# Performance work log

Measured on AMD Instinct MI355X. Metric: run time of the kernel, lower is better.

The kernel has to match this reference:

```python
import math
import jax, jax.numpy as jnp
import numpy as np

N_TOKENS = 2048
HIDDEN = 2880
HEAD_DIM = 64
N_HEADS = 64          # total attention heads
N_KV = 8              # key/value heads
Q_MULT = N_HEADS // N_KV
SLIDING_WINDOW = 128  # layer_idx=0 (even) -> window active
ROPE_BASE = 150000.0
INIT_CTX = 4096.0
ROPE_SCALE = 32.0
NTK_ALPHA = 1.0
NTK_BETA = 32.0
QKV_DIM = HEAD_DIM * (N_HEADS + 2 * N_KV)  # 5120
EPS = 1e-5
NEG = -1e30


def _cos_sin(n_tokens):
    # YaRN-scaled rotary tables (scaling_factor > 1 branch)
    freq = ROPE_BASE ** (jnp.arange(0, HEAD_DIM, 2, dtype=jnp.float32) / HEAD_DIM)
    concentration = 0.1 * jnp.log(jnp.float32(ROPE_SCALE)) + 1.0
    d_half = HEAD_DIM / 2
    log_base = jnp.log(jnp.float32(ROPE_BASE))
    low = d_half * jnp.log(jnp.float32(INIT_CTX / (NTK_BETA * 2 * np.pi))) / log_base
    high = d_half * jnp.log(jnp.float32(INIT_CTX / (NTK_ALPHA * 2 * np.pi))) / log_base
    interpolation = 1.0 / (ROPE_SCALE * freq)
    extrapolation = 1.0 / freq
    ramp = (jnp.arange(d_half, dtype=jnp.float32) - low) / (high - low)
    mask = 1.0 - jnp.clip(ramp, 0.0, 1.0)
    inv_freq = interpolation * (1.0 - mask) + extrapolation * mask
    t = jnp.arange(n_tokens, dtype=jnp.float32)
    freqs = t[:, None] * inv_freq[None, :]          # [n, head_dim//2]
    return jnp.cos(freqs) * concentration, jnp.sin(freqs) * concentration


def _apply_rotary(x, cos, sin):
    # x: [n, heads, head_dim]; cos/sin: [n, head_dim//2]
    cos = cos[:, None, :].astype(x.dtype)
    sin = sin[:, None, :].astype(x.dtype)
    x1, x2 = jnp.split(x, 2, axis=-1)
    return jnp.concatenate((x1 * cos - x2 * sin, x2 * cos + x1 * sin), axis=-1)


def _rmsnorm(x, scale):
    t = x.astype(jnp.float32)
    rms = jnp.sqrt(jnp.mean(t * t, axis=-1, keepdims=True) + EPS)
    return (t / rms * scale).astype(x.dtype)


def _sdpa(q, k, v, sinks):
    # q: [n, h_kv, q_mult, d]; k, v: [n, h_kv, d]; sinks: [n_heads]
    n = q.shape[0]
    sm_scale = 1.0 / math.sqrt(HEAD_DIM)
    q32, k32, v32 = q.astype(jnp.float32), k.astype(jnp.float32), v.astype(jnp.float32)
    qk = jnp.einsum('qhmd,khd->hmqk', q32, k32) * jnp.float32(sm_scale)
    i = jnp.arange(n)
    # causal AND within sliding window: q - window < k <= q
    allowed = (i[None, :] <= i[:, None]) & (i[None, :] > i[:, None] - SLIDING_WINDOW)
    qk = qk + jnp.where(allowed, jnp.float32(0.0), jnp.float32(NEG))[None, None, :, :]
    s = sinks.astype(jnp.float32).reshape(N_KV, Q_MULT, 1, 1)
    s = jnp.broadcast_to(s, (N_KV, Q_MULT, n, 1))
    w = jax.nn.softmax(jnp.concatenate([qk, s], axis=-1), axis=-1)[..., :-1]
    attn = jnp.einsum('hmqk,khd->qhmd', w, v32)
    return attn.astype(q.dtype).reshape(n, -1)  # [n, n_heads*head_dim]


def setup_inputs() -> dict:
    key = jax.random.key(0)
    ks = jax.random.split(key, 5)
    s = 0.02
    return {
        'x': jax.random.normal(ks[0], (N_TOKENS, HIDDEN), jnp.float32),
        'norm_scale': jnp.ones((HIDDEN,), jnp.float32),
        'w_qkv': jax.random.normal(ks[1], (HIDDEN, QKV_DIM), jnp.float32) * s,
        'b_qkv': jnp.zeros((QKV_DIM,), jnp.float32),
        'sinks': jax.random.normal(ks[2], (N_HEADS,), jnp.float32),
        'w_out': jax.random.normal(ks[3], (N_HEADS * HEAD_DIM, HIDDEN), jnp.float32) * s,
        'b_out': jnp.zeros((HIDDEN,), jnp.float32),
    }


def reference(x, norm_scale, w_qkv, b_qkv, sinks, w_out, b_out):
    n = x.shape[0]
    t = _rmsnorm(x, norm_scale)
    qkv = t @ w_qkv + b_qkv                                   # [n, qkv_dim]
    q_end = N_HEADS * HEAD_DIM
    k_end = q_end + N_KV * HEAD_DIM
    q = qkv[:, :q_end].reshape(n, N_KV, Q_MULT, HEAD_DIM)
    k = qkv[:, q_end:k_end].reshape(n, N_KV, HEAD_DIM)
    v = qkv[:, k_end:].reshape(n, N_KV, HEAD_DIM)
    cos, sin = _cos_sin(n)
    q = _apply_rotary(q.reshape(n, -1, HEAD_DIM), cos, sin).reshape(n, N_KV, Q_MULT, HEAD_DIM)
    k = _apply_rotary(k, cos, sin)
    attn = _sdpa(q, k, v, sinks)                              # [n, n_heads*head_dim]
    return x + (attn @ w_out + b_out)
```

## Files before the change

### kernel.cpp

```cpp
#include <hip/hip_runtime.h>
#include <hip/hip_bf16.h>
#include <math.h>

#define N_TOK 2048
#define HIDDEN 2880
#define QKV_DIM 5120
#define LOG2E 1.44269504088896340736f

typedef __attribute__((ext_vector_type(8))) short short8;
typedef __attribute__((ext_vector_type(4))) float f32x4;
typedef __attribute__((ext_vector_type(16))) float f32x16;

__device__ __forceinline__ float bf2f(unsigned short u) {
  union { unsigned int i; float f; } c; c.i = ((unsigned int)u) << 16; return c.f;
}
__device__ __forceinline__ unsigned short f2bf(float f) {
  union { float f; unsigned int i; } c; c.f = f;
  unsigned int i = c.i;
  return (unsigned short)((i + 0x7FFFu + ((i >> 16) & 1u)) >> 16);
}
__device__ __forceinline__ void gload16(const void* g, void* l) {
  __builtin_amdgcn_global_load_lds((const __attribute__((address_space(1))) void*)g,
                                   (__attribute__((address_space(3))) void*)l, 16, 0, 0);
}

__global__ __launch_bounds__(256) void prep1_kernel(
    const float* __restrict__ w_qkv, unsigned short* __restrict__ wqkvT,
    const float* __restrict__ x, const float* __restrict__ scale,
    unsigned short* __restrict__ t_bf,
    float* __restrict__ cstab, float* __restrict__ sntab)
{
  __shared__ float tile[64][65];
  int b = blockIdx.x;
  const int t = threadIdx.x;
  if (b >= 5648) {
    const float log_base = 11.9183905731f;
    const float low  = 32.f * logf(4096.f / (32.f * 6.283185307179586f)) / log_base;
    const float high = 32.f * logf(4096.f / 6.283185307179586f) / log_base;
    const float conc = 1.3465735903f;
    int e0 = (b - 5648) * 1024 + t * 4;
#pragma unroll
    for (int k = 0; k < 4; ++k) {
      int entry = e0 + k;
      int token = entry >> 5, d = entry & 31;
      float fj = (float)d;
      float extrap = expf(-log_base * fj * 0.03125f);
      float interp = extrap * 0.03125f;
      float ramp = (fj - low) / (high - low);
      float maskv = 1.f - fminf(fmaxf(ramp, 0.f), 1.f);
      float inv_freq = interp * (1.f - maskv) + extrap * maskv;
      float ang = (float)token * inv_freq;
      float s, c;
      sincosf(ang, &s, &c);
      cstab[entry] = c * conc;
      sntab[entry] = s * conc;
    }
    return;
  }
  if (b >= 3600) {
    int row = b - 3600;
    const float* xr = x + (size_t)row * HIDDEN;
    float ss = 0.f;
    for (int i = t; i < HIDDEN / 4; i += 256) {
      float4 v = ((const float4*)xr)[i];
      ss += v.x * v.x + v.y * v.y + v.z * v.z + v.w * v.w;
    }
#pragma unroll
    for (int off = 32; off; off >>= 1) ss += __shfl_down(ss, off, 64);
    __shared__ float red[4];
    if ((t & 63) == 0) red[t >> 6] = ss;
    __syncthreads();
    float total = red[0] + red[1] + red[2] + red[3];
    float rinv = rsqrtf(total / (float)HIDDEN + 1e-5f);
    for (int i = t; i < HIDDEN / 4; i += 256) {
      float4 v = ((const float4*)xr)[i];
      float4 s4 = ((const float4*)scale)[i];
      union { unsigned short u[4]; uint2 p; } pk;
      pk.u[0] = f2bf(v.x * rinv * s4.x);
      pk.u[1] = f2bf(v.y * rinv * s4.y);
      pk.u[2] = f2bf(v.z * rinv * s4.z);
      pk.u[3] = f2bf(v.w * rinv * s4.w);
      *(uint2*)&t_bf[(size_t)row * HIDDEN + i * 4] = pk.p;
    }
    return;
  }
  int bx = b % 80, by = b / 80;
  const int r0 = by * 64, c0 = bx * 64;
  const int c4 = t & 15, rr = t >> 4;
#pragma unroll
  for (int p = 0; p < 4; ++p) {
    int row = rr + p * 16;
    float4 v = *(const float4*)&w_qkv[(size_t)(r0 + row) * 5120 + c0 + c4 * 4];
    tile[row][c4 * 4 + 0] = v.x; tile[row][c4 * 4 + 1] = v.y;
    tile[row][c4 * 4 + 2] = v.z; tile[row][c4 * 4 + 3] = v.w;
  }
  __syncthreads();
  const int rc = t & 7;
#pragma unroll
  for (int it = 0; it < 2; ++it) {
    int cc = (t >> 3) + it * 32;
    unsigned short tmp[8];
#pragma unroll
    for (int i = 0; i < 8; ++i) tmp[i] = f2bf(tile[rc * 8 + i][cc]);
    *(uint4*)&wqkvT[(size_t)(c0 + cc) * 2880 + r0 + rc * 8] = *(uint4*)tmp;
  }
}

template <int NF, int EPI>
__global__ __launch_bounds__(512, 2) void gemm8(
    const unsigned short* __restrict__ A,
    const unsigned short* __restrict__ Bt,
    const float* __restrict__ bias,
    const float* __restrict__ resid,
    void* __restrict__ Cout,
    int K, int Ncols)
{
  constexpr int BUFSZ = 16384 + NF * 8192;
  constexpr int NCH = 2 + NF;
  constexpr int HALF = NCH / 2;
  __shared__ char smem_[2 * BUFSZ];
  const int tid = threadIdx.x;
  const int lane = tid & 63;
  const int w = tid >> 6;
  const int fr = lane & 15, fq = lane >> 4;
  const int wr = w >> 2, wc = w & 3;

  const int nwg = gridDim.x;
  const int cpx = nwg >> 3;
  const int wg = (blockIdx.x & 7) * cpx + (blockIdx.x >> 3);
  const int by = wg & 15, bx = wg >> 4;
  const int row0 = by * 128, col0 = bx * (NF * 64);

  const unsigned short* gsrc[NCH];
  int ldsoff[NCH];
#pragma unroll
  for (int c = 0; c < NCH; ++c) {
    int g = tid + 512 * c;
    if (g < 1024) {
      int kk = g >> 9, rr = (g >> 2) & 127, u = g & 3;
      gsrc[c] = A + (size_t)(row0 + rr) * K + kk * 32 + ((u ^ ((rr >> 1) & 3)) * 8);
      ldsoff[c] = kk * 8192 + rr * 64 + u * 16;
    } else {
      int g2 = g - 1024;
      int kk = g2 / (NF * 256);
      int rm = g2 - kk * (NF * 256);
      int rr = rm >> 2, u = rm & 3;
      gsrc[c] = Bt + (size_t)(col0 + rr) * K + kk * 32 + ((u ^ ((rr >> 1) & 3)) * 8);
      ldsoff[c] = 16384 + kk * (NF * 4096) + rr * 64 + u * 16;
    }
  }
  const int urd = (fq ^ ((fr >> 1) & 3)) * 16;
  const int aoffb = (wr * 64 + fr) * 64 + urd;
  const int boffb = 16384 + (wc * NF * 16 + fr) * 64 + urd;

  f32x4 acc[4][NF];
#pragma unroll
  for (int mf = 0; mf < 4; ++mf)
#pragma unroll
    for (int nf = 0; nf < NF; ++nf) acc[mf][nf] = (f32x4)0.f;

  const int NT = K >> 6;

#define ISSUE(c) gload16(gsrc[c] + ktn, smem_ + nbufo + ldsoff[c])
#define RD_A(mf, kk) (*(const short8*)(smem_ + bufo + (kk)*8192 + (mf)*1024 + aoffb))
#define RD_B(nf, kk) (*(const short8*)(smem_ + bufo + (kk)*(NF*4096) + (nf)*1024 + boffb))

  {
    const int ktn = 0, nbufo = 0;
#pragma unroll
    for (int c = 0; c < NCH; ++c) gload16(gsrc[c] + ktn, smem_ + nbufo + ldsoff[c]);
  }

  for (int t = 0; t < NT; ++t) {
    const int bufo = (t & 1) * BUFSZ;
    const int nbufo = bufo ^ BUFSZ;
    const int ktn = (t + 1) * 64;
    const bool pref = (t + 1) < NT;

    asm volatile("s_waitcnt vmcnt(0)" ::: "memory");
    __builtin_amdgcn_s_barrier();

    if (pref) {
#pragma unroll
      for (int c = 0; c < HALF; ++c) ISSUE(c);
    }

    short8 afr[4], bfr[NF];
#pragma unroll
    for (int nf = 0; nf < NF; ++nf) bfr[nf] = RD_B(nf, 0);
#pragma unroll
    for (int mf = 0; mf < 4; ++mf) afr[mf] = RD_A(mf, 0);
    __builtin_amdgcn_s_setprio(1);
#pragma unroll
    for (int mf = 0; mf < 4; ++mf)
#pragma unroll
      for (int nf = 0; nf < NF; ++nf)
        acc[mf][nf] = __builtin_amdgcn_mfma_f32_16x16x32_bf16(afr[mf], bfr[nf], acc[mf][nf], 0, 0, 0);
    __builtin_amdgcn_s_setprio(0);

    if (pref) {
#pragma unroll
      for (int c = HALF; c < NCH; ++c) ISSUE(c);
    }

#pragma unroll
    for (int nf = 0; nf < NF; ++nf) bfr[nf] = RD_B(nf, 1);
#pragma unroll
    for (int mf = 0; mf < 4; ++mf) afr[mf] = RD_A(mf, 1);
    __builtin_amdgcn_s_setprio(1);
#pragma unroll
    for (int mf = 0; mf < 4; ++mf)
#pragma unroll
      for (int nf = 0; nf < NF; ++nf)
        acc[mf][nf] = __builtin_amdgcn_mfma_f32_16x16x32_bf16(afr[mf], bfr[nf], acc[mf][nf], 0, 0, 0);
    __builtin_amdgcn_s_setprio(0);
  }
#undef ISSUE
#undef RD_A
#undef RD_B

#pragma unroll
  for (int mf = 0; mf < 4; ++mf) {
#pragma unroll
    for (int nf = 0; nf < NF; ++nf) {
      const int colb = col0 + wc * NF * 16 + nf * 16 + fr;
      const int rowb = row0 + wr * 64 + mf * 16 + fq * 4;
      const float bs = bias[colb];
      if (EPI == 1) {
#pragma unroll
        for (int j = 0; j < 4; ++j)
          ((unsigned short*)Cout)[(size_t)(rowb + j) * Ncols + colb] =
              f2bf(acc[mf][nf][j] + bs);
      } else {
#pragma unroll
        for (int j = 0; j < 4; ++j) {
          const size_t idx = (size_t)(rowb + j) * Ncols + colb;
          ((float*)Cout)[idx] = acc[mf][nf][j] + bs + resid[idx];
        }
      }
    }
  }
}

__global__ __launch_bounds__(512, 2) void gemm_o(
    const unsigned short* __restrict__ A,
    const unsigned short* __restrict__ Bt,
    const float* __restrict__ bias,
    const float* __restrict__ resid,
    float* __restrict__ Cout,
    int K, int Ncols)
{
  constexpr int NF = 3;
  constexpr int BUFSZ = 32768 + NF * 16384;
  __shared__ char smem_[2 * BUFSZ];
  const int tid = threadIdx.x;
  const int lane = tid & 63;
  const int w = tid >> 6;
  const int fr = lane & 15, fq = lane >> 4;
  const int wr = w >> 2, wc = w & 3;

  const int nwg = gridDim.x;
  const int cpx = nwg >> 3;
  const int wg = (blockIdx.x & 7) * cpx + (blockIdx.x >> 3);
  const int by = wg & 15, bx = wg >> 4;
  const int row0 = by * 128, col0 = bx * (NF * 64);

  const unsigned short* gsrcA[4];
  int loffA[4];
#pragma unroll
  for (int c = 0; c < 4; ++c) {
    int g = tid + 512 * c;
    int kk = g >> 9, rr = (g >> 2) & 127, u = g & 3;
    gsrcA[c] = A + (size_t)(row0 + rr) * K + kk * 32 + ((u ^ ((rr >> 1) & 3)) * 8);
    loffA[c] = kk * 8192 + rr * 64 + u * 16;
  }
  const unsigned short* gsrcB[6];
  int loffB[6];
#pragma unroll
  for (int c = 0; c < 6; ++c) {
    int g = tid + 512 * c;
    int kk = g / 768;
    int rm = g - kk * 768;
    int rr = rm >> 2, u = rm & 3;
    gsrcB[c] = Bt + (size_t)(col0 + rr) * K + kk * 32 + ((u ^ ((rr >> 1) & 3)) * 8);
    loffB[c] = 32768 + kk * 12288 + rr * 64 + u * 16;
  }
  const int urd = (fq ^ ((fr >> 1) & 3)) * 16;
  const int aoffb = (wr * 64 + fr) * 64 + urd;
  const int boffb = 32768 + (wc * 48 + fr) * 64 + urd;

  f32x4 acc[4][NF];
#pragma unroll
  for (int mf = 0; mf < 4; ++mf)
#pragma unroll
    for (int nf = 0; nf < NF; ++nf) acc[mf][nf] = (f32x4)0.f;

  const int NT = K >> 7;

#define RD_A(mf, kk) (*(const short8*)(smem_ + bufo + (kk)*8192 + (mf)*1024 + aoffb))
#define RD_B(nf, kk) (*(const short8*)(smem_ + bufo + (kk)*12288 + (nf)*1024 + boffb))

#pragma unroll
  for (int c = 0; c < 4; ++c) gload16(gsrcA[c], smem_ + loffA[c]);
#pragma unroll
  for (int c = 0; c < 6; ++c) gload16(gsrcB[c], smem_ + loffB[c]);

  for (int t = 0; t < NT; ++t) {
    const int bufo = (t & 1) * BUFSZ;
    const int nbufo = bufo ^ BUFSZ;
    const int ktn = (t + 1) * 128;
    const bool pref = (t + 1) < NT;

    asm volatile("s_waitcnt vmcnt(0)" ::: "memory");
    __builtin_amdgcn_s_barrier();

    if (pref) {
#pragma unroll
      for (int c = 0; c < 4; ++c) gload16(gsrcA[c] + ktn, smem_ + nbufo + loffA[c]);
      gload16(gsrcB[0] + ktn, smem_ + nbufo + loffB[0]);
    }

    short8 afr[4], bfr[NF];
#pragma unroll
    for (int kk = 0; kk < 4; ++kk) {
#pragma unroll
      for (int nf = 0; nf < NF; ++nf) bfr[nf] = RD_B(nf, kk);
#pragma unroll
      for (int mf = 0; mf < 4; ++mf) afr[mf] = RD_A(mf, kk);
      __builtin_amdgcn_s_setprio(1);
#pragma unroll
      for (int mf = 0; mf < 4; ++mf)
#pragma unroll
        for (int nf = 0; nf < NF; ++nf)
          acc[mf][nf] = __builtin_amdgcn_mfma_f32_16x16x32_bf16(afr[mf], bfr[nf], acc[mf][nf], 0, 0, 0);
      __builtin_amdgcn_s_setprio(0);
      if (kk == 0 && pref) {
#pragma unroll
        for (int c = 1; c < 6; ++c) gload16(gsrcB[c] + ktn, smem_ + nbufo + loffB[c]);
      }
    }
  }
#undef RD_A
#undef RD_B

#pragma unroll
  for (int mf = 0; mf < 4; ++mf) {
#pragma unroll
    for (int nf = 0; nf < NF; ++nf) {
      const int colb = col0 + wc * NF * 16 + nf * 16 + fr;
      const int rowb = row0 + wr * 64 + mf * 16 + fq * 4;
      const float bs = bias[colb];
#pragma unroll
      for (int j = 0; j < 4; ++j) {
        const size_t idx = (size_t)(rowb + j) * Ncols + colb;
        Cout[idx] = acc[mf][nf][j] + bs + resid[idx];
      }
    }
  }
}

__global__ __launch_bounds__(512) void attn_trans_kernel(
    const unsigned short* __restrict__ qkv, const float* __restrict__ sinks,
    const float* __restrict__ cstab, const float* __restrict__ sntab,
    unsigned short* __restrict__ attn,
    const float* __restrict__ w_out, unsigned short* __restrict__ woutT)
{
  __shared__ char smem[45056];
  const int tid = threadIdx.x;
  int bb = blockIdx.x;
  if (bb >= 512) {
    int b = bb - 512;
    int bx = b % 45, by = b / 45;
    const int r0 = by * 64, c0 = bx * 64;
    float (*tile)[65] = (float(*)[65])smem;
    const int c4 = tid & 15, rr = tid >> 4;
#pragma unroll
    for (int p = 0; p < 2; ++p) {
      int row = rr + p * 32;
      float4 v = *(const float4*)&w_out[(size_t)(r0 + row) * 2880 + c0 + c4 * 4];
      tile[row][c4 * 4 + 0] = v.x; tile[row][c4 * 4 + 1] = v.y;
      tile[row][c4 * 4 + 2] = v.z; tile[row][c4 * 4 + 3] = v.w;
    }
    __syncthreads();
    const int rc = tid & 7, cc = tid >> 3;
    unsigned short tmp[8];
#pragma unroll
    for (int i = 0; i < 8; ++i) tmp[i] = f2bf(tile[rc * 8 + i][cc]);
    *(uint4*)&woutT[(size_t)(c0 + cc) * 4096 + r0 + rc * 8] = *(uint4*)tmp;
    return;
  }
  unsigned short* Ks = (unsigned short*)smem;
  unsigned short* Vt = (unsigned short*)(smem + 20480);
  const int lane = tid & 63;
  const int w    = tid >> 6;
  const int qb = bb & 63, kvh = bb >> 6;
  const int q0 = qb * 32;
  const int kb = q0 - 128;
  const int h  = lane >> 5;
  const int ql = lane & 31;

  for (int task = tid; task < 640; task += 512) {
    int r = task >> 2, p = task & 3;
    int j = kb + r; if (j < 0) j = 0;
    const unsigned short* kp = qkv + (size_t)j * QKV_DIM + 4096 + kvh * 64 + p * 8;
    short8 klo = *(const short8*)kp;
    short8 khi = *(const short8*)(kp + 32);
    float cv[8], sv[8];
    *(float4*)&cv[0] = *(const float4*)&cstab[j * 32 + p * 8];
    *(float4*)&cv[4] = *(const float4*)&cstab[j * 32 + p * 8 + 4];
    *(float4*)&sv[0] = *(const float4*)&sntab[j * 32 + p * 8];
    *(float4*)&sv[4] = *(const float4*)&sntab[j * 32 + p * 8 + 4];
    unsigned short nlo[8], nhi[8];
#pragma unroll
    for (int e = 0; e < 8; ++e) {
      float lo = bf2f(((const unsigned short*)&klo)[e]);
      float hi = bf2f(((const unsigned short*)&khi)[e]);
      nlo[e] = f2bf(lo * cv[e] - hi * sv[e]);
      nhi[e] = f2bf(hi * cv[e] + lo * sv[e]);
    }
    *(short8*)&Ks[r * 64 + ((p ^ (r & 7)) * 8)]       = *(short8*)nlo;
    *(short8*)&Ks[r * 64 + (((p + 4) ^ (r & 7)) * 8)] = *(short8*)nhi;
  }
  for (int c = tid; c < 2560; c += 512) {
    int jl = c >> 4;
    int d4 = (c & 15) * 4;
    int j = kb + jl; if (j < 0) j = 0;
    ushort4 v4 = *(const ushort4*)&qkv[(size_t)j * QKV_DIM + 4608 + kvh * 64 + d4];
    const unsigned short* pv = (const unsigned short*)&v4;
#pragma unroll
    for (int t = 0; t < 4; ++t) {
      int d = d4 + t;
      int slot = (jl >> 3) ^ (d & 7);
      Vt[d * 192 + slot * 8 + (jl & 7)] = pv[t];
    }
  }
  const int head = kvh * 8 + w;
  const int i_q = q0 + ql;
  short8 qf[4];
  {
    const unsigned short* qp = qkv + (size_t)i_q * QKV_DIM + head * 64 + h * 8;
#pragma unroll
    for (int ks = 0; ks < 4; ++ks) qf[ks] = *(const short8*)(qp + ks * 16);
#pragma unroll
    for (int p = 0; p < 2; ++p) {
      float cv[8], sv[8];
      int o = i_q * 32 + p * 16 + h * 8;
      *(float4*)&cv[0] = *(const float4*)&cstab[o];
      *(float4*)&cv[4] = *(const float4*)&cstab[o + 4];
      *(float4*)&sv[0] = *(const float4*)&sntab[o];
      *(float4*)&sv[4] = *(const float4*)&sntab[o + 4];
      unsigned short nlo[8], nhi[8];
#pragma unroll
      for (int e = 0; e < 8; ++e) {
        float lo = bf2f(((const unsigned short*)&qf[p])[e]);
        float hi = bf2f(((const unsigned short*)&qf[p + 2])[e]);
        nlo[e] = f2bf(lo * cv[e] - hi * sv[e]);
        nhi[e] = f2bf(hi * cv[e] + lo * sv[e]);
      }
      qf[p]     = *(short8*)nlo;
      qf[p + 2] = *(short8*)nhi;
    }
  }
  __syncthreads();

  const float SC = 0.125f * LOG2E;
  f32x16 oacc0 = (f32x16)(0.f), oacc1 = (f32x16)(0.f);
  float m = -1e30f, l = 0.f;

  const int tstart = qb < 4 ? 4 - qb : 0;
  for (int tt = tstart; tt < 5; ++tt) {
    const int j0 = kb + tt * 32;
    f32x16 sacc = (f32x16)(0.f);
    const int kr = tt * 32 + ql;
#pragma unroll
    for (int ks = 0; ks < 4; ++ks) {
      short8 kf = *(const short8*)&Ks[kr * 64 + (((ks * 2 + h) ^ (kr & 7)) * 8)];
      sacc = __builtin_amdgcn_mfma_f32_32x32x16_bf16(kf, qf[ks], sacc, 0, 0, 0);
    }
    float sc16[16];
    float mt = -INFINITY;
#pragma unroll
    for (int e = 0; e < 16; ++e) {
      int kk = (e & 3) + 8 * (e >> 2) + 4 * h;
      int j = j0 + kk;
      float s2 = sacc[e] * SC;
      bool valid = (j <= i_q) && (j > i_q - 128);
      s2 = valid ? s2 : -INFINITY;
      sc16[e] = s2;
      mt = fmaxf(mt, s2);
    }
    mt = fmaxf(mt, __shfl_xor(mt, 32));
    float mnew = fmaxf(m, mt);
    float r = exp2f(m - mnew);
    l *= r;
    oacc0 *= r;
    oacc1 *= r;
    m = mnew;
    unsigned int wpk[8];
    float ls = 0.f;
#pragma unroll
    for (int e2 = 0; e2 < 8; ++e2) {
      float plo = exp2f(sc16[2 * e2]     - m);
      float phi = exp2f(sc16[2 * e2 + 1] - m);
      ls += plo + phi;
      asm("v_cvt_pk_bf16_f32 %0, %1, %2" : "=v"(wpk[e2]) : "v"(plo), "v"(phi));
    }
    l += ls;
#pragma unroll
    for (int m16 = 0; m16 < 2; ++m16) {
      int go = 2 * m16 + h;
      int gs = 2 * m16 + 1 - h;
      unsigned int x0 = (unsigned int)__shfl_xor((int)wpk[2 * gs],     32);
      unsigned int x1 = (unsigned int)__shfl_xor((int)wpk[2 * gs + 1], 32);
      union { unsigned int u[4]; short8 s; } bu;
      bu.u[0] = h ? x0 : wpk[2 * go];
      bu.u[1] = h ? x1 : wpk[2 * go + 1];
      bu.u[2] = h ? wpk[2 * go]     : x0;
      bu.u[3] = h ? wpk[2 * go + 1] : x1;
      short8 bfrag = bu.s;
#pragma unroll
      for (int dt = 0; dt < 2; ++dt) {
        int d = dt * 32 + ql;
        int slot = (tt * 4 + m16 * 2 + h) ^ (d & 7);
        short8 vf = *(const short8*)&Vt[d * 192 + slot * 8];
        if (dt == 0)
          oacc0 = __builtin_amdgcn_mfma_f32_32x32x16_bf16(vf, bfrag, oacc0, 0, 0, 0);
        else
          oacc1 = __builtin_amdgcn_mfma_f32_32x32x16_bf16(vf, bfrag, oacc1, 0, 0, 0);
      }
    }
  }
  float lt = l + __shfl_xor(l, 32);
  lt += exp2f(sinks[head] * LOG2E - m);
  float inv = 1.f / lt;
  unsigned short* op = attn + (size_t)i_q * 4096 + head * 64;
#pragma unroll
  for (int dt = 0; dt < 2; ++dt) {
#pragma unroll
    for (int g = 0; g < 4; ++g) {
      float f0, f1, f2, f3;
      if (dt == 0) {
        f0 = oacc0[4 * g]; f1 = oacc0[4 * g + 1]; f2 = oacc0[4 * g + 2]; f3 = oacc0[4 * g + 3];
      } else {
        f0 = oacc1[4 * g]; f1 = oacc1[4 * g + 1]; f2 = oacc1[4 * g + 2]; f3 = oacc1[4 * g + 3];
      }
      unsigned int u0, u1;
      asm("v_cvt_pk_bf16_f32 %0, %1, %2" : "=v"(u0) : "v"(f0 * inv), "v"(f1 * inv));
      asm("v_cvt_pk_bf16_f32 %0, %1, %2" : "=v"(u1) : "v"(f2 * inv), "v"(f3 * inv));
      int d = dt * 32 + 8 * g + 4 * h;
      uint2 pr; pr.x = u0; pr.y = u1;
      *(uint2*)(op + d) = pr;
    }
  }
}

extern "C" void kernel_launch(void* const* d_in, const int* in_sizes, int n_in,
                              void* d_out, int out_size, void* d_ws, size_t ws_size,
                              hipStream_t stream)
{
  const float* x      = (const float*)d_in[0];
  const float* nscale = (const float*)d_in[1];
  const float* w_qkv  = (const float*)d_in[2];
  const float* b_qkv  = (const float*)d_in[3];
  const float* sinks  = (const float*)d_in[4];
  const float* w_out  = (const float*)d_in[5];
  const float* b_out  = (const float*)d_in[6];

  char* ws = (char*)d_ws;
  unsigned short* t_bf  = (unsigned short*)(ws);
  unsigned short* wqkvT = (unsigned short*)(ws + 11796480);
  unsigned short* qkv   = (unsigned short*)(ws + 41287680);
  unsigned short* attn  = (unsigned short*)(ws + 62259200);
  unsigned short* woutT = (unsigned short*)(ws + 79036416);
  float* cstab          = (float*)(ws + 102629376);
  float* sntab          = (float*)(ws + 102891520);

  prep1_kernel<<<5712, 256, 0, stream>>>(w_qkv, wqkvT, x, nscale, t_bf, cstab, sntab);
  gemm8<5, 1><<<256, 512, 0, stream>>>(t_bf, wqkvT, b_qkv, nullptr, (void*)qkv, 2880, 5120);
  attn_trans_kernel<<<3392, 512, 0, stream>>>(qkv, sinks, cstab, sntab, attn, w_out, woutT);
  gemm_o<<<240, 512, 0, stream>>>(attn, woutT, b_out, x, (float*)d_out, 4096, 2880);
}
```

Baseline: 172.6 us.

## Give each wave private LDS tiles to drop workgroup barriers in QKV GEMM

Replaces the shared double-buffered QKV GEMM with a per-wave private-LDS design. Each of the 8 waves loads its own 64x64 A slice and 80x64 B slice into a dedicated 18 KB LDS region, so the block-wide s_barrier goes away. Each wave reads its fragments into registers, then issues the next tile's loads before running its MFMAs. The cost is 144 KB of LDS per block, which limits occupancy to one block per CU, and no data is shared across waves, so global/L2 traffic rises and there is no double buffering.

```diff
diff --git a/kernel.cpp b/kernel.cpp
--- a/kernel.cpp
+++ b/kernel.cpp
@@ -106,19 +106,14 @@
   }
 }
 
-template <int NF, int EPI>
-__global__ __launch_bounds__(512, 2) void gemm8(
+__global__ __launch_bounds__(512, 1) void gemm_wp(
     const unsigned short* __restrict__ A,
     const unsigned short* __restrict__ Bt,
     const float* __restrict__ bias,
-    const float* __restrict__ resid,
-    void* __restrict__ Cout,
+    unsigned short* __restrict__ Cout,
     int K, int Ncols)
 {
-  constexpr int BUFSZ = 16384 + NF * 8192;
-  constexpr int NCH = 2 + NF;
-  constexpr int HALF = NCH / 2;
-  __shared__ char smem_[2 * BUFSZ];
+  __shared__ char smem_[147456];
   const int tid = threadIdx.x;
   const int lane = tid & 63;
   const int w = tid >> 6;
@@ -129,115 +124,87 @@
   const int cpx = nwg >> 3;
   const int wg = (blockIdx.x & 7) * cpx + (blockIdx.x >> 3);
   const int by = wg & 15, bx = wg >> 4;
-  const int row0 = by * 128, col0 = bx * (NF * 64);
-
-  const unsigned short* gsrc[NCH];
-  int ldsoff[NCH];
-#pragma unroll
-  for (int c = 0; c < NCH; ++c) {
-    int g = tid + 512 * c;
-    if (g < 1024) {
-      int kk = g >> 9, rr = (g >> 2) & 127, u = g & 3;
-      gsrc[c] = A + (size_t)(row0 + rr) * K + kk * 32 + ((u ^ ((rr >> 1) & 3)) * 8);
-      ldsoff[c] = kk * 8192 + rr * 64 + u * 16;
-    } else {
-      int g2 = g - 1024;
-      int kk = g2 / (NF * 256);
-      int rm = g2 - kk * (NF * 256);
-      int rr = rm >> 2, u = rm & 3;
-      gsrc[c] = Bt + (size_t)(col0 + rr) * K + kk * 32 + ((u ^ ((rr >> 1) & 3)) * 8);
-      ldsoff[c] = 16384 + kk * (NF * 4096) + rr * 64 + u * 16;
-    }
-  }
+  const int arow0 = by * 128 + wr * 64;
+  const int bcol0 = bx * 320 + wc * 80;
+  const int wb = w * 18432;
+
+  int offA[8], offB[10];
+#pragma unroll
+  for (int c = 0; c < 8; ++c) {
+    int g = c * 64 + lane;
+    int kk = g >> 8, rem = g & 255, rr = rem >> 2, u = rem & 3;
+    offA[c] = (arow0 + rr) * K + kk * 32 + ((u ^ ((rr >> 1) & 3)) * 8);
+  }
+#pragma unroll
+  for (int c = 0; c < 10; ++c) {
+    int g = c * 64 + lane;
+    int kk = g / 320, rem = g - kk * 320, rr = rem >> 2, u = rem & 3;
+    offB[c] = (bcol0 + rr) * K + kk * 32 + ((u ^ ((rr >> 1) & 3)) * 8);
+  }
+  const int ldsA = wb + lane * 16;
+  const int ldsB = wb + 8192 + lane * 16;
   const int urd = (fq ^ ((fr >> 1) & 3)) * 16;
-  const int aoffb = (wr * 64 + fr) * 64 + urd;
-  const int boffb = 16384 + (wc * NF * 16 + fr) * 64 + urd;
-
-  f32x4 acc[4][NF];
+  const int aoff = wb + fr * 64 + urd;
+  const int boff = wb + 8192 + fr * 64 + urd;
+
+  f32x4 acc[4][5];
 #pragma unroll
   for (int mf = 0; mf < 4; ++mf)
 #pragma unroll
-    for (int nf = 0; nf < NF; ++nf) acc[mf][nf] = (f32x4)0.f;
+    for (int nf = 0; nf < 5; ++nf) acc[mf][nf] = (f32x4)0.f;
 
   const int NT = K >> 6;
 
-#define ISSUE(c) gload16(gsrc[c] + ktn, smem_ + nbufo + ldsoff[c])
-#define RD_A(mf, kk) (*(const short8*)(smem_ + bufo + (kk)*8192 + (mf)*1024 + aoffb))
-#define RD_B(nf, kk) (*(const short8*)(smem_ + bufo + (kk)*(NF*4096) + (nf)*1024 + boffb))
-
-  {
-    const int ktn = 0, nbufo = 0;
-#pragma unroll
-    for (int c = 0; c < NCH; ++c) gload16(gsrc[c] + ktn, smem_ + nbufo + ldsoff[c]);
-  }
+#pragma unroll
+  for (int c = 0; c < 8; ++c)  gload16(A + offA[c], smem_ + ldsA + c * 1024);
+#pragma unroll
+  for (int c = 0; c < 10; ++c) gload16(Bt + offB[c], smem_ + ldsB + c * 1024);
 
   for (int t = 0; t < NT; ++t) {
-    const int bufo = (t & 1) * BUFSZ;
-    const int nbufo = bufo ^ BUFSZ;
     const int ktn = (t + 1) * 64;
-    const bool pref = (t + 1) < NT;
-
     asm volatile("s_waitcnt vmcnt(0)" ::: "memory");
-    __builtin_amdgcn_s_barrier();
-
-    if (pref) {
-#pragma unroll
-      for (int c = 0; c < HALF; ++c) ISSUE(c);
-    }
-
-    short8 afr[4], bfr[NF];
-#pragma unroll
-    for (int nf = 0; nf < NF; ++nf) bfr[nf] = RD_B(nf, 0);
-#pragma unroll
-    for (int mf = 0; mf < 4; ++mf) afr[mf] = RD_A(mf, 0);
+
+    short8 fa[4][2], fb[5][2];
+#pragma unroll
+    for (int kk = 0; kk < 2; ++kk) {
+#pragma unroll
+      for (int mf = 0; mf < 4; ++mf)
+        fa[mf][kk] = *(const short8*)(smem_ + aoff + kk * 4096 + mf * 1024);
+#pragma unroll
+      for (int nf = 0; nf < 5; ++nf)
+        fb[nf][kk] = *(const short8*)(smem_ + boff + kk * 5120 + nf * 1024);
+    }
+    asm volatile("s_waitcnt lgkmcnt(0)" ::: "memory");
+    __builtin_amdgcn_sched_barrier(0);
+
+    if (t + 1 < NT) {
+#pragma unroll
+      for (int c = 0; c < 8; ++c)  gload16(A + offA[c] + ktn, smem_ + ldsA + c * 1024);
+#pragma unroll
+      for (int c = 0; c < 10; ++c) gload16(Bt + offB[c] + ktn, smem_ + ldsB + c * 1024);
+    }
+
     __builtin_amdgcn_s_setprio(1);
 #pragma unroll
-    for (int mf = 0; mf < 4; ++mf)
-#pragma unroll
-      for (int nf = 0; nf < NF; ++nf)
-        acc[mf][nf] = __builtin_amdgcn_mfma_f32_16x16x32_bf16(afr[mf], bfr[nf], acc[mf][nf], 0, 0, 0);
+    for (int kk = 0; kk < 2; ++kk)
+#pragma unroll
+      for (int mf = 0; mf < 4; ++mf)
+#pragma unroll
+        for (int nf = 0; nf < 5; ++nf)
+          acc[mf][nf] = __builtin_amdgcn_mfma_f32_16x16x32_bf16(fa[mf][kk], fb[nf][kk], acc[mf][nf], 0, 0, 0);
     __builtin_amdgcn_s_setprio(0);
-
-    if (pref) {
-#pragma unroll
-      for (int c = HALF; c < NCH; ++c) ISSUE(c);
-    }
-
-#pragma unroll
-    for (int nf = 0; nf < NF; ++nf) bfr[nf] = RD_B(nf, 1);
-#pragma unroll
-    for (int mf = 0; mf < 4; ++mf) afr[mf] = RD_A(mf, 1);
-    __builtin_amdgcn_s_setprio(1);
-#pragma unroll
-    for (int mf = 0; mf < 4; ++mf)
-#pragma unroll
-      for (int nf = 0; nf < NF; ++nf)
-        acc[mf][nf] = __builtin_amdgcn_mfma_f32_16x16x32_bf16(afr[mf], bfr[nf], acc[mf][nf], 0, 0, 0);
-    __builtin_amdgcn_s_setprio(0);
-  }
-#undef ISSUE
-#undef RD_A
-#undef RD_B
+  }
 
 #pragma unroll
   for (int mf = 0; mf < 4; ++mf) {
 #pragma unroll
-    for (int nf = 0; nf < NF; ++nf) {
-      const int colb = col0 + wc * NF * 16 + nf * 16 + fr;
-      const int rowb = row0 + wr * 64 + mf * 16 + fq * 4;
+    for (int nf = 0; nf < 5; ++nf) {
+      const int colb = bcol0 + nf * 16 + fr;
+      const int rowb = arow0 + mf * 16 + fq * 4;
       const float bs = bias[colb];
-      if (EPI == 1) {
-#pragma unroll
-        for (int j = 0; j < 4; ++j)
-          ((unsigned short*)Cout)[(size_t)(rowb + j) * Ncols + colb] =
-              f2bf(acc[mf][nf][j] + bs);
-      } else {
-#pragma unroll
-        for (int j = 0; j < 4; ++j) {
-          const size_t idx = (size_t)(rowb + j) * Ncols + colb;
-          ((float*)Cout)[idx] = acc[mf][nf][j] + bs + resid[idx];
-        }
-      }
+#pragma unroll
+      for (int j = 0; j < 4; ++j)
+        Cout[(size_t)(rowb + j) * Ncols + colb] = f2bf(acc[mf][nf][j] + bs);
     }
   }
 }
@@ -576,7 +543,7 @@
   float* sntab          = (float*)(ws + 102891520);
 
   prep1_kernel<<<5712, 256, 0, stream>>>(w_qkv, wqkvT, x, nscale, t_bf, cstab, sntab);
-  gemm8<5, 1><<<256, 512, 0, stream>>>(t_bf, wqkvT, b_qkv, nullptr, (void*)qkv, 2880, 5120);
+  gemm_wp<<<256, 512, 0, stream>>>(t_bf, wqkvT, b_qkv, qkv, 2880, 5120);
   attn_trans_kernel<<<3392, 512, 0, stream>>>(qkv, sinks, cstab, sntab, attn, w_out, woutT);
   gemm_o<<<240, 512, 0, stream>>>(attn, woutT, b_out, x, (float*)d_out, 4096, 2880);
 }
```

After: 191.6 us. 1.11x slower.
